# Performance work log

Measured on AMD Instinct MI355X. Metric: run time of the kernel, lower is better.

Reference implementation:

```python
import jax, jax.numpy as jnp
import numpy as np

N, D_IN = 65536, 512
H1, H2, D_SH = 1024, 1024, 512   # shared net: num_nodes_shared = [1024, 1024, 512]
HI = 512                          # indiv hidden width, num_nodes_indiv = [512, 512]


def setup_inputs() -> dict:
    key = jax.random.key(0)
    ks = jax.random.split(key, 16)
    s = 0.02
    inp = {
        "input": jax.random.normal(ks[0], (N, D_IN), jnp.float32),
        "treatment": jax.random.randint(ks[1], (N,), 0, 2, jnp.int32),
        # shared net (hidden ReLU layers + linear output, all with bias)
        "W0": jax.random.normal(ks[2], (D_IN, H1), jnp.float32) * s,
        "b0": jnp.zeros((H1,), jnp.float32),
        "W1": jax.random.normal(ks[3], (H1, H2), jnp.float32) * s,
        "b1": jnp.zeros((H2,), jnp.float32),
        "W2": jax.random.normal(ks[4], (H2, D_SH), jnp.float32) * s,
        "b2": jnp.zeros((D_SH,), jnp.float32),
        # risk net 0 (output layer has no bias)
        "A0": jax.random.normal(ks[5], (D_SH, HI), jnp.float32) * s,
        "a0": jnp.zeros((HI,), jnp.float32),
        "A1": jax.random.normal(ks[6], (HI, HI), jnp.float32) * s,
        "a1": jnp.zeros((HI,), jnp.float32),
        "A2": jax.random.normal(ks[7], (HI, 1), jnp.float32) * s,
        # risk net 1
        "C0": jax.random.normal(ks[8], (D_SH, HI), jnp.float32) * s,
        "c0": jnp.zeros((HI,), jnp.float32),
        "C1": jax.random.normal(ks[9], (HI, HI), jnp.float32) * s,
        "c1": jnp.zeros((HI,), jnp.float32),
        "C2": jax.random.normal(ks[10], (HI, 1), jnp.float32) * s,
    }
    return inp


def _risk_net(h, U0, u0, U1, u1, U2):
    h = jax.nn.relu(h @ U0 + u0)
    h = jax.nn.relu(h @ U1 + u1)
    return h @ U2  # [N, 1], no output bias


def reference(input, treatment, W0, b0, W1, b1, W2, b2,
              A0, a0, A1, a1, A2, C0, c0, C1, c1, C2):
    # shared MLP
    h = jax.nn.relu(input @ W0 + b0)
    h = jax.nn.relu(h @ W1 + b1)
    out = h @ W2 + b2                     # [N, D_SH]
    # Binary expert routing. The torch code gathers samples per treatment,
    # runs each group through its own MLP and scatters results back; the
    # math is equivalent to applying both experts and selecting per sample.
    y0 = _risk_net(out, A0, a0, A1, a1, A2)[:, 0]  # [N]
    y1 = _risk_net(out, C0, c0, C1, c1, C2)[:, 0]  # [N]
    y = jnp.where(treatment == 0, y0, y1)          # [N]
    return (y, out)
```

## Files before the change

kernel.cpp:

```cpp
#include <hip/hip_runtime.h>
#include <hip/hip_bf16.h>
#include <stdint.h>

typedef short short8 __attribute__((ext_vector_type(8)));
typedef float f32x4 __attribute__((ext_vector_type(4)));

#define NSAMP 65536
#define AS1 __attribute__((address_space(1)))
#define AS3 __attribute__((address_space(3)))

__device__ __forceinline__ unsigned f2bf(float f) {
    union { float f; unsigned u; } v; v.f = f;
    unsigned u = v.u;
    u += 0x7fffu + ((u >> 16) & 1u);
    return u >> 16;
}


__global__ void k_convert_bf16(const float* __restrict__ in, unsigned short* __restrict__ out, int n8) {
    int i = blockIdx.x * blockDim.x + threadIdx.x;
    if (i >= n8) return;
    const float4* p = (const float4*)in + (size_t)i * 2;
    float4 a = p[0], b = p[1];
    short8 o;
    o[0] = (short)f2bf(a.x); o[1] = (short)f2bf(a.y);
    o[2] = (short)f2bf(a.z); o[3] = (short)f2bf(a.w);
    o[4] = (short)f2bf(b.x); o[5] = (short)f2bf(b.y);
    o[6] = (short)f2bf(b.z); o[7] = (short)f2bf(b.w);
    ((short8*)out)[i] = o;
}

struct PrepArgs {
    const float *W0, *W1, *W2, *A0, *C0, *A1, *C1, *a0v, *c0v;
    unsigned short *W0T, *W1T, *W2T, *RT0, *A1T, *C1T;
    float *bcat, *yout;
};
__global__ void k_prep(PrepArgs p) {
    int i = blockIdx.x * blockDim.x + threadIdx.x;
    if (i < 524288)  { int k = i >> 10, n = i & 1023; p.W0T[n * 512 + k] = f2bf(p.W0[i]); return; }
    i -= 524288;
    if (i < 1048576) { int k = i >> 10, n = i & 1023; p.W1T[n * 1024 + k] = f2bf(p.W1[i]); return; }
    i -= 1048576;
    if (i < 524288)  { int k = i >> 9, n = i & 511; p.W2T[n * 1024 + k] = f2bf(p.W2[i]); return; }
    i -= 524288;
    if (i < 262144)  { int k = i >> 9, n = i & 511; p.RT0[n * 512 + k] = f2bf(p.A0[i]); return; }
    i -= 262144;
    if (i < 262144)  { int k = i >> 9, n = i & 511; p.RT0[(512 + n) * 512 + k] = f2bf(p.C0[i]); return; }
    i -= 262144;
    if (i < 262144)  { int k = i >> 9, n = i & 511; p.A1T[n * 512 + k] = f2bf(p.A1[i]); return; }
    i -= 262144;
    if (i < 262144)  { int k = i >> 9, n = i & 511; p.C1T[n * 512 + k] = f2bf(p.C1[i]); return; }
    i -= 262144;
    if (i < 512)     { p.bcat[i] = p.a0v[i]; return; }
    i -= 512;
    if (i < 512)     { p.bcat[512 + i] = p.c0v[i]; return; }
    i -= 512;
    if (i < 65536)   { p.yout[i] = 0.f; return; }
}

template<int MODE>
__global__ __launch_bounds__(512, 2)
void k_gemm256(const unsigned short* __restrict__ A, int lda,
               const unsigned short* __restrict__ BT, const unsigned short* __restrict__ BT2,
               const float* __restrict__ bias, const float* __restrict__ bias2,
               unsigned short* __restrict__ Cbf, float* __restrict__ Cf32,
               const float* __restrict__ w2, const float* __restrict__ w2b,
               const int* __restrict__ TRt, float* __restrict__ ydot,
               int Ncols, int K, int TPB)
{
    __shared__ __align__(16) char lds[131072];

    const int tid  = threadIdx.x;
    const int lane = tid & 63;
    const int wid  = tid >> 6;
    const int wr   = wid >> 2;
    const int wcn  = wid & 3;
    const int m0   = blockIdx.x << 8;

    const int srow = tid >> 2;
    const int scs  = (tid & 3) ^ ((srow >> 1) & 3);
    const int ldst = wid * 1024;

    auto mk = [&](int tau, const unsigned short*& a0, const unsigned short*& a1,
                  const unsigned short*& b0, const unsigned short*& b1) {
        int cOff = 0;
        int n0e = tau << 8;
        const unsigned short* Bsel = BT;
        if (MODE == 2) {
            int expert = tau >> 1;
            n0e = (tau & 1) << 8;
            cOff = expert << 9;
            if (expert) Bsel = BT2;
        }
        a0 = A + (size_t)(m0 + srow) * lda + cOff + scs * 8;
        a1 = a0 + (size_t)128 * lda;
        b0 = Bsel + (size_t)(n0e + srow) * K + scs * 8;
        b1 = b0 + (size_t)128 * K;
    };

#define STAGE_BLK(dbuf, blkoff, g0, g1, koff)                                            \
    do {                                                                                 \
        __builtin_amdgcn_global_load_lds((const AS1 void*)((g0) + (koff)),               \
                                         (AS3 void*)((dbuf) + (blkoff) + ldst), 16, 0, 0); \
        __builtin_amdgcn_global_load_lds((const AS1 void*)((g1) + (koff)),               \
                                         (AS3 void*)((dbuf) + (blkoff) + 8192 + ldst), 16, 0, 0); \
    } while (0)

    int aOff[8], bOff[4];
#pragma unroll
    for (int i = 0; i < 8; ++i) {
        int r = wr * 128 + i * 16 + (lane & 15);
        aOff[i] = r * 64 + ((((lane >> 4) ^ ((r >> 1) & 3))) << 4);
    }
#pragma unroll
    for (int j = 0; j < 4; ++j) {
        int r = wcn * 64 + j * 16 + (lane & 15);
        bOff[j] = r * 64 + ((((lane >> 4) ^ ((r >> 1) & 3))) << 4);
    }

    f32x4 acc[8][4];
#pragma unroll
    for (int i = 0; i < 8; ++i)
#pragma unroll
        for (int j = 0; j < 4; ++j) acc[i][j] = (f32x4)0.f;

    const int KT  = K >> 6;
    const int TOT = TPB * KT;

    const unsigned short *cA0, *cA1, *cB0, *cB1;
    mk(0, cA0, cA1, cB0, cB1);
    const unsigned short *nA0 = cA0, *nA1 = cA1, *nB0 = cB0, *nB1 = cB1;

    STAGE_BLK(lds, 0,     cA0, cA1, 0);
    STAGE_BLK(lds, 32768, cB0, cB1, 0);
    STAGE_BLK(lds, 16384, cA0, cA1, 32);
    STAGE_BLK(lds, 49152, cB0, cB1, 32);
    asm volatile("s_waitcnt vmcnt(4)" ::: "memory");
    __builtin_amdgcn_s_barrier();

    int g = 0;
    for (int tau = 0; tau < TPB; ++tau) {
        if (tau + 1 < TPB) mk(tau + 1, nA0, nA1, nB0, nB1);

        for (int t = 0; t < KT; ++t, ++g) {
            const char* sbuf = lds + (g & 1) * 65536;
            char* dbuf = lds + ((g + 1) & 1) * 65536;
            const bool inTile = (t + 1 < KT);
            const bool st = (g + 1 < TOT);
            const unsigned short* sA0 = inTile ? cA0 : nA0;
            const unsigned short* sA1 = inTile ? cA1 : nA1;
            const unsigned short* sB0 = inTile ? cB0 : nB0;
            const unsigned short* sB1 = inTile ? cB1 : nB1;
            const int koff = inTile ? ((t + 1) << 6) : 0;
            short8 af[4], bfv[4];

#pragma unroll
            for (int i = 0; i < 4; ++i) af[i]  = *(const short8*)(sbuf + aOff[i]);
#pragma unroll
            for (int j = 0; j < 4; ++j) bfv[j] = *(const short8*)(sbuf + 32768 + bOff[j]);
            if (st) STAGE_BLK(dbuf, 0, sA0, sA1, koff);
            __builtin_amdgcn_s_barrier();
            asm volatile("s_waitcnt lgkmcnt(0)" ::: "memory");
            __builtin_amdgcn_sched_barrier(0);
            __builtin_amdgcn_s_setprio(1);
#pragma unroll
            for (int i = 0; i < 4; ++i)
#pragma unroll
                for (int j = 0; j < 4; ++j)
                    acc[i][j] = __builtin_amdgcn_mfma_f32_16x16x32_bf16(bfv[j], af[i], acc[i][j], 0, 0, 0);
            __builtin_amdgcn_s_setprio(0);
            __builtin_amdgcn_s_barrier();

#pragma unroll
            for (int i = 0; i < 4; ++i) af[i] = *(const short8*)(sbuf + aOff[4 + i]);
            if (st) STAGE_BLK(dbuf, 32768, sB0, sB1, koff);
            __builtin_amdgcn_s_barrier();
            asm volatile("s_waitcnt lgkmcnt(0)" ::: "memory");
            __builtin_amdgcn_sched_barrier(0);
            __builtin_amdgcn_s_setprio(1);
#pragma unroll
            for (int i = 0; i < 4; ++i)
#pragma unroll
                for (int j = 0; j < 4; ++j)
                    acc[4 + i][j] = __builtin_amdgcn_mfma_f32_16x16x32_bf16(bfv[j], af[i], acc[4 + i][j], 0, 0, 0);
            __builtin_amdgcn_s_setprio(0);
            if (st) { asm volatile("s_waitcnt vmcnt(4)" ::: "memory"); }
            else    { asm volatile("s_waitcnt vmcnt(0)" ::: "memory"); }
            __builtin_amdgcn_sched_barrier(0);
            __builtin_amdgcn_s_barrier();

#pragma unroll
            for (int i = 0; i < 4; ++i) af[i]  = *(const short8*)(sbuf + 16384 + aOff[i]);
#pragma unroll
            for (int j = 0; j < 4; ++j) bfv[j] = *(const short8*)(sbuf + 49152 + bOff[j]);
            if (st) STAGE_BLK(dbuf, 16384, sA0, sA1, koff + 32);
            __builtin_amdgcn_s_barrier();
            asm volatile("s_waitcnt lgkmcnt(0)" ::: "memory");
            __builtin_amdgcn_sched_barrier(0);
            __builtin_amdgcn_s_setprio(1);
#pragma unroll
            for (int i = 0; i < 4; ++i)
#pragma unroll
                for (int j = 0; j < 4; ++j)
                    acc[i][j] = __builtin_amdgcn_mfma_f32_16x16x32_bf16(bfv[j], af[i], acc[i][j], 0, 0, 0);
            __builtin_amdgcn_s_setprio(0);
            __builtin_amdgcn_s_barrier();

#pragma unroll
            for (int i = 0; i < 4; ++i) af[i] = *(const short8*)(sbuf + 16384 + aOff[4 + i]);
            if (st) STAGE_BLK(dbuf, 49152, sB0, sB1, koff + 32);
            __builtin_amdgcn_s_barrier();
            asm volatile("s_waitcnt lgkmcnt(0)" ::: "memory");
            __builtin_amdgcn_sched_barrier(0);
            __builtin_amdgcn_s_setprio(1);
#pragma unroll
            for (int i = 0; i < 4; ++i)
#pragma unroll
                for (int j = 0; j < 4; ++j)
                    acc[4 + i][j] = __builtin_amdgcn_mfma_f32_16x16x32_bf16(bfv[j], af[i], acc[4 + i][j], 0, 0, 0);
            __builtin_amdgcn_s_setprio(0);
            if (st) { asm volatile("s_waitcnt vmcnt(4)" ::: "memory"); }
            __builtin_amdgcn_sched_barrier(0);
            __builtin_amdgcn_s_barrier();
        }

        if (MODE == 2) {
            const int expert = tau >> 1;
            const int n0e = (tau & 1) << 8;
            const float* be = expert ? bias2 : bias;
            const float* we = expert ? w2b : w2;
            const int nb = n0e + wcn * 64 + ((lane >> 4) << 2);
            f32x4 bv[4], wv[4];
#pragma unroll
            for (int j = 0; j < 4; ++j) {
                bv[j] = *(const f32x4*)(be + nb + j * 16);
                wv[j] = *(const f32x4*)(we + nb + j * 16);
            }
#pragma unroll
            for (int i = 0; i < 8; ++i) {
                float p = 0.f;
#pragma unroll
                for (int j = 0; j < 4; ++j)
#pragma unroll
                    for (int r = 0; r < 4; ++r)
                        p += fmaxf(acc[i][j][r] + bv[j][r], 0.f) * wv[j][r];
                p += __shfl_xor(p, 16);
                p += __shfl_xor(p, 32);
                const int m = m0 + wr * 128 + i * 16 + (lane & 15);
                if (lane < 16 && TRt[m] == expert) atomicAdd(&ydot[m], p);
            }
        } else {
            const int n0e = tau << 8;
            const int nb = n0e + wcn * 64 + ((lane >> 4) << 2);
            f32x4 bv[4];
#pragma unroll
            for (int j = 0; j < 4; ++j) bv[j] = *(const f32x4*)(bias + nb + j * 16);
#pragma unroll
            for (int i = 0; i < 8; ++i) {
                const int m = m0 + wr * 128 + i * 16 + (lane & 15);
                unsigned short* pb = Cbf + (size_t)m * Ncols + nb;
#pragma unroll
                for (int j = 0; j < 4; ++j) {
                    f32x4 v = acc[i][j] + bv[j];
                    if (MODE == 0) {
#pragma unroll
                        for (int r = 0; r < 4; ++r) v[r] = fmaxf(v[r], 0.f);
                    }
                    if (MODE == 1) *(f32x4*)(Cf32 + (size_t)m * Ncols + nb + j * 16) = v;
                    unsigned long long pk =
                        (unsigned long long)(f2bf(v[0]) | (f2bf(v[1]) << 16)) |
                        ((unsigned long long)(f2bf(v[2]) | (f2bf(v[3]) << 16)) << 32);
                    *(unsigned long long*)(pb + j * 16) = pk;
                }
            }
        }

#pragma unroll
        for (int i = 0; i < 8; ++i)
#pragma unroll
            for (int j = 0; j < 4; ++j) acc[i][j] = (f32x4)0.f;
        cA0 = nA0; cA1 = nA1; cB0 = nB0; cB1 = nB1;
    }
#undef STAGE_BLK
}


extern "C" void kernel_launch(void* const* d_in, const int* in_sizes, int n_in,
                              void* d_out, int out_size, void* d_ws, size_t ws_size,
                              hipStream_t stream) {
    const float* X  = (const float*)d_in[0];
    const int*  TR  = (const int*)d_in[1];
    const float* W0 = (const float*)d_in[2];  const float* b0 = (const float*)d_in[3];
    const float* W1 = (const float*)d_in[4];  const float* b1 = (const float*)d_in[5];
    const float* W2 = (const float*)d_in[6];  const float* b2 = (const float*)d_in[7];
    const float* A0 = (const float*)d_in[8];  const float* a0 = (const float*)d_in[9];
    const float* A1 = (const float*)d_in[10]; const float* a1 = (const float*)d_in[11];
    const float* A2 = (const float*)d_in[12];
    const float* C0 = (const float*)d_in[13]; const float* c0 = (const float*)d_in[14];
    const float* C1 = (const float*)d_in[15]; const float* c1 = (const float*)d_in[16];
    const float* C2 = (const float*)d_in[17];

    float* y_out   = (float*)d_out;
    float* out_out = (float*)d_out + NSAMP;

    char* ws = (char*)d_ws;
    size_t off = 0;
    auto alloc = [&](size_t bytes) -> char* {
        char* p = ws + off;
        off += (bytes + 255) & ~(size_t)255;
        return p;
    };
    unsigned short* Xb  = (unsigned short*)alloc((size_t)NSAMP * 512 * 2);
    unsigned short* H1b = (unsigned short*)alloc((size_t)NSAMP * 1024 * 2);
    unsigned short* H2b = (unsigned short*)alloc((size_t)NSAMP * 1024 * 2);
    unsigned short* OUTb = H1b;
    unsigned short* R01  = H2b;
    unsigned short* W0T = (unsigned short*)alloc(512 * 1024 * 2);
    unsigned short* W1T = (unsigned short*)alloc(1024 * 1024 * 2);
    unsigned short* W2T = (unsigned short*)alloc(1024 * 512 * 2);
    unsigned short* RT0 = (unsigned short*)alloc(1024 * 512 * 2);
    unsigned short* A1T = (unsigned short*)alloc(512 * 512 * 2);
    unsigned short* C1T = (unsigned short*)alloc(512 * 512 * 2);
    float* bcat = (float*)alloc(1024 * 4);

    k_convert_bf16<<<(NSAMP * 512 / 8 + 255) / 256, 256, 0, stream>>>(X, Xb, NSAMP * 512 / 8);
    PrepArgs pa;
    pa.W0 = W0; pa.W1 = W1; pa.W2 = W2; pa.A0 = A0; pa.C0 = C0; pa.A1 = A1; pa.C1 = C1;
    pa.a0v = a0; pa.c0v = c0;
    pa.W0T = W0T; pa.W1T = W1T; pa.W2T = W2T; pa.RT0 = RT0; pa.A1T = A1T; pa.C1T = C1T;
    pa.bcat = bcat; pa.yout = y_out;
    k_prep<<<(3212288 + 255) / 256, 256, 0, stream>>>(pa);

    k_gemm256<0><<<256, 512, 0, stream>>>(Xb, 512, W0T, nullptr, b0, nullptr,
                                          H1b, nullptr, nullptr, nullptr, nullptr, nullptr,
                                          1024, 512, 4);
    k_gemm256<0><<<256, 512, 0, stream>>>(H1b, 1024, W1T, nullptr, b1, nullptr,
                                          H2b, nullptr, nullptr, nullptr, nullptr, nullptr,
                                          1024, 1024, 4);
    k_gemm256<1><<<256, 512, 0, stream>>>(H2b, 1024, W2T, nullptr, b2, nullptr,
                                          OUTb, out_out, nullptr, nullptr, nullptr, nullptr,
                                          512, 1024, 2);

    k_gemm256<0><<<256, 512, 0, stream>>>(OUTb, 512, RT0, nullptr, bcat, nullptr,
                                          R01, nullptr, nullptr, nullptr, nullptr, nullptr,
                                          1024, 512, 4);

    k_gemm256<2><<<256, 512, 0, stream>>>(R01, 1024, A1T, C1T, a1, c1,
                                          nullptr, nullptr, A2, C2, TR, y_out,
                                          512, 512, 4);
}
```

Measured before the change: 622.7 us.

## Reassign persistent GEMM blocks to fixed column tile iterating over row tiles

Each persistent block used to own one 256-row slab of A and sweep all column tiles (or expert tiles). Now a block is pinned to one column tile of B (and one expert) and strides over several row tiles, with a swizzled block id that spreads blocks across XCDs. Keeping B fixed per block is meant to improve L2 reuse of the weight tiles and to simplify address generation. A rows are now re-read by several blocks rather than once per block. The change assumes a grid of 256 blocks and that TPB divides 256.

Measured after the change: 575.3 us. -7.6%, faster.

```diff
diff --git a/kernel.cpp b/kernel.cpp
--- a/kernel.cpp
+++ b/kernel.cpp
@@ -75,28 +75,32 @@
     const int wid  = tid >> 6;
     const int wr   = wid >> 2;
     const int wcn  = wid & 3;
-    const int m0   = blockIdx.x << 8;
+
+    const int bid = (int)((blockIdx.x & 7) * 32 + (blockIdx.x >> 3));
+    const int cls = bid % TPB;
+    const int w   = bid / TPB;
+    const int MSTEP = 256 / TPB;
+
+    int n0e, cOff = 0, expert = 0;
+    const unsigned short* Bsel = BT;
+    if (MODE == 2) {
+        expert = cls >> 1;
+        n0e = (cls & 1) << 8;
+        cOff = expert << 9;
+        if (expert) Bsel = BT2;
+    } else {
+        n0e = cls << 8;
+    }
 
     const int srow = tid >> 2;
     const int scs  = (tid & 3) ^ ((srow >> 1) & 3);
     const int ldst = wid * 1024;
 
-    auto mk = [&](int tau, const unsigned short*& a0, const unsigned short*& a1,
-                  const unsigned short*& b0, const unsigned short*& b1) {
-        int cOff = 0;
-        int n0e = tau << 8;
-        const unsigned short* Bsel = BT;
-        if (MODE == 2) {
-            int expert = tau >> 1;
-            n0e = (tau & 1) << 8;
-            cOff = expert << 9;
-            if (expert) Bsel = BT2;
-        }
-        a0 = A + (size_t)(m0 + srow) * lda + cOff + scs * 8;
-        a1 = a0 + (size_t)128 * lda;
-        b0 = Bsel + (size_t)(n0e + srow) * K + scs * 8;
-        b1 = b0 + (size_t)128 * K;
-    };
+    const unsigned short* gB0 = Bsel + (size_t)(n0e + srow) * K + scs * 8;
+    const unsigned short* gB1 = gB0 + (size_t)128 * K;
+    const size_t dA = (size_t)MSTEP * 256 * lda;
+    const unsigned short* cA0 = A + (size_t)((w << 8) + srow) * lda + cOff + scs * 8;
+    const unsigned short* cA1 = cA0 + (size_t)128 * lda;
 
 #define STAGE_BLK(dbuf, blkoff, g0, g1, koff)                                            \
     do {                                                                                 \
@@ -127,20 +131,17 @@
     const int KT  = K >> 6;
     const int TOT = TPB * KT;
 
-    const unsigned short *cA0, *cA1, *cB0, *cB1;
-    mk(0, cA0, cA1, cB0, cB1);
-    const unsigned short *nA0 = cA0, *nA1 = cA1, *nB0 = cB0, *nB1 = cB1;
-
     STAGE_BLK(lds, 0,     cA0, cA1, 0);
-    STAGE_BLK(lds, 32768, cB0, cB1, 0);
+    STAGE_BLK(lds, 32768, gB0, gB1, 0);
     STAGE_BLK(lds, 16384, cA0, cA1, 32);
-    STAGE_BLK(lds, 49152, cB0, cB1, 32);
+    STAGE_BLK(lds, 49152, gB0, gB1, 32);
     asm volatile("s_waitcnt vmcnt(4)" ::: "memory");
     __builtin_amdgcn_s_barrier();
 
     int g = 0;
     for (int tau = 0; tau < TPB; ++tau) {
-        if (tau + 1 < TPB) mk(tau + 1, nA0, nA1, nB0, nB1);
+        const unsigned short* nA0 = cA0 + dA;
+        const unsigned short* nA1 = cA1 + dA;
 
         for (int t = 0; t < KT; ++t, ++g) {
             const char* sbuf = lds + (g & 1) * 65536;
@@ -149,8 +150,6 @@
             const bool st = (g + 1 < TOT);
             const unsigned short* sA0 = inTile ? cA0 : nA0;
             const unsigned short* sA1 = inTile ? cA1 : nA1;
-            const unsigned short* sB0 = inTile ? cB0 : nB0;
-            const unsigned short* sB1 = inTile ? cB1 : nB1;
             const int koff = inTile ? ((t + 1) << 6) : 0;
             short8 af[4], bfv[4];
 
@@ -173,7 +172,7 @@
 
 #pragma unroll
             for (int i = 0; i < 4; ++i) af[i] = *(const short8*)(sbuf + aOff[4 + i]);
-            if (st) STAGE_BLK(dbuf, 32768, sB0, sB1, koff);
+            if (st) STAGE_BLK(dbuf, 32768, gB0, gB1, koff);
             __builtin_amdgcn_s_barrier();
             asm volatile("s_waitcnt lgkmcnt(0)" ::: "memory");
             __builtin_amdgcn_sched_barrier(0);
@@ -208,7 +207,7 @@
 
 #pragma unroll
             for (int i = 0; i < 4; ++i) af[i] = *(const short8*)(sbuf + 16384 + aOff[4 + i]);
-            if (st) STAGE_BLK(dbuf, 49152, sB0, sB1, koff + 32);
+            if (st) STAGE_BLK(dbuf, 49152, gB0, gB1, koff + 32);
             __builtin_amdgcn_s_barrier();
             asm volatile("s_waitcnt lgkmcnt(0)" ::: "memory");
             __builtin_amdgcn_sched_barrier(0);
@@ -224,9 +223,8 @@
             __builtin_amdgcn_s_barrier();
         }
 
+        const int m0 = (w + MSTEP * tau) << 8;
         if (MODE == 2) {
-            const int expert = tau >> 1;
-            const int n0e = (tau & 1) << 8;
             const float* be = expert ? bias2 : bias;
             const float* we = expert ? w2b : w2;
             const int nb = n0e + wcn * 64 + ((lane >> 4) << 2);
@@ -250,7 +248,6 @@
                 if (lane < 16 && TRt[m] == expert) atomicAdd(&ydot[m], p);
             }
         } else {
-            const int n0e = tau << 8;
             const int nb = n0e + wcn * 64 + ((lane >> 4) << 2);
             f32x4 bv[4];
 #pragma unroll
@@ -279,7 +276,7 @@
         for (int i = 0; i < 8; ++i)
 #pragma unroll
             for (int j = 0; j < 4; ++j) acc[i][j] = (f32x4)0.f;
-        cA0 = nA0; cA1 = nA1; cB0 = nB0; cB1 = nB1;
+        cA0 = nA0; cA1 = nA1;
     }
 #undef STAGE_BLK
 }
```
